# Optimization experiments

Measured on AMD Instinct MI355X. Metric: run time of the kernel, lower is better.

## Reference

```python
import jax, jax.numpy as jnp
import numpy as np

B, F, P, H = 8192, 32, 512, 256
EPS_W = 1e-8   # weight-normalization eps from _normalize_weights
EPS_LN = 1e-5  # torch LayerNorm default eps


def setup_inputs() -> dict:
    key = jax.random.key(0)
    k0, k1, k2, k3, k4 = jax.random.split(key, 5)
    phys = jax.random.normal(k0, (B, F, P), dtype=jnp.float32)
    ratios = jax.random.uniform(k1, (B, F), dtype=jnp.float32)
    lengths = jax.random.randint(k2, (B,), 1, F + 1, dtype=jnp.int32)
    ln_gamma = jnp.ones((P,), jnp.float32)
    ln_beta = jnp.zeros((P,), jnp.float32)
    lim1 = float(np.sqrt(6.0 / (P + H)))  # xavier_uniform
    W1 = jax.random.uniform(k3, (H, P), jnp.float32, -lim1, lim1)
    b1 = jnp.zeros((H,), jnp.float32)
    lim2 = float(np.sqrt(6.0 / (H + 1)))
    W2 = jax.random.uniform(k4, (1, H), jnp.float32, -lim2, lim2)
    b2 = jnp.zeros((1,), jnp.float32)
    return dict(phys=phys, ratios=ratios, lengths=lengths,
                ln_gamma=ln_gamma, ln_beta=ln_beta,
                W1=W1, b1=b1, W2=W2, b2=b2)


def reference(phys, ratios, lengths, ln_gamma, ln_beta, W1, b1, W2, b2):
    # Ragged weighted mix: mask padded fragments, normalize weights per sample.
    mask = (jnp.arange(F)[None, :] < lengths[:, None]).astype(phys.dtype)  # [B,F]
    w = ratios * mask
    w = w / (jnp.sum(w, axis=-1, keepdims=True) + EPS_W)
    mix = jnp.einsum('bf,bfp->bp', w, phys)  # [B,P]
    # Head: LayerNorm(P) -> Linear(P,H) -> ReLU -> Linear(H,1)
    mu = jnp.mean(mix, axis=-1, keepdims=True)
    var = jnp.mean((mix - mu) ** 2, axis=-1, keepdims=True)
    xn = (mix - mu) * jax.lax.rsqrt(var + EPS_LN) * ln_gamma + ln_beta
    h = jax.nn.relu(xn @ W1.T + b1)  # [B,H]
    y = h @ W2.T + b2                # [B,1]
    return jnp.nan_to_num(y)
```

## Files before the change

kernel.cpp:

```cpp
#include <hip/hip_runtime.h>
#include <math.h>

#define BB 8192
#define FF 32
#define PP 512
#define HH 256
#define S  16

__global__ void transpose_w1(const float* __restrict__ W1, float* __restrict__ W1T) {
    int p = blockIdx.x;
    int j = threadIdx.x;
    W1T[((p >> 2) * HH + j) * 4 + (p & 3)] = W1[j * PP + p];
}

__global__ __launch_bounds__(256, 2)
void fused_physchem(const float* __restrict__ phys,
                    const float* __restrict__ ratios,
                    const int*   __restrict__ lengths,
                    const float* __restrict__ gamma,
                    const float* __restrict__ beta,
                    const float* __restrict__ W1T,
                    const float* __restrict__ b1,
                    const float* __restrict__ W2,
                    const float* __restrict__ b2,
                    float* __restrict__ out) {
    constexpr int PADP = PP + 4;
    __shared__ float wts[S][FF];
    __shared__ int   slen[S];
    __shared__ __align__(16) float xn[S][PADP];
    __shared__ float red[4][8][2];

    const int tid  = threadIdx.x;
    const int wave = tid >> 6;
    const int lane = tid & 63;
    const int b0   = blockIdx.x * S;

    {
        int g = tid >> 5;
        int f = tid & 31;
        #pragma unroll
        for (int rep = 0; rep < 2; ++rep) {
            int s = g + 8 * rep;
            int len = lengths[b0 + s];
            float r = ratios[(b0 + s) * FF + f];
            float w = (f < len) ? r : 0.0f;
            float sum = w;
            #pragma unroll
            for (int m = 16; m >= 1; m >>= 1) sum += __shfl_xor(sum, m, 32);
            wts[s][f] = w / (sum + 1e-8f);
            if (f == 0) slen[s] = len;
        }
    }
    __syncthreads();

    const int pt = tid & 127;
    const int sh = tid >> 7;
    float4 mixacc[8];
    {
        const float4* phys4 = (const float4*)phys;
        #pragma unroll
        for (int k = 0; k < 8; ++k) {
            const int s   = 2 * k + sh;
            const int len = slen[s];
            const float4* row = phys4 + (size_t)(b0 + s) * FF * (PP / 4) + pt;
            float4 a = make_float4(0.f, 0.f, 0.f, 0.f);
            #pragma unroll 8
            for (int f = 0; f < len; ++f) {
                float  w = wts[s][f];
                float4 v = row[(size_t)f * (PP / 4)];
                a.x += w * v.x; a.y += w * v.y;
                a.z += w * v.z; a.w += w * v.w;
            }
            mixacc[k] = a;
        }
    }

    #pragma unroll
    for (int k = 0; k < 8; ++k) {
        float4 a = mixacc[k];
        float sum = a.x + a.y + a.z + a.w;
        float sq  = a.x * a.x + a.y * a.y + a.z * a.z + a.w * a.w;
        #pragma unroll
        for (int m = 32; m >= 1; m >>= 1) {
            sum += __shfl_xor(sum, m, 64);
            sq  += __shfl_xor(sq,  m, 64);
        }
        if (lane == 0) { red[wave][k][0] = sum; red[wave][k][1] = sq; }
    }
    __syncthreads();
    {
        float4 g  = ((const float4*)gamma)[pt];
        float4 be = ((const float4*)beta)[pt];
        const int wbase = sh * 2;
        #pragma unroll
        for (int k = 0; k < 8; ++k) {
            const int s = 2 * k + sh;
            float sum = red[wbase][k][0] + red[wbase + 1][k][0];
            float sq  = red[wbase][k][1] + red[wbase + 1][k][1];
            float mu  = sum * (1.0f / PP);
            float var = sq * (1.0f / PP) - mu * mu;
            float inv = rsqrtf(var + 1e-5f);
            float4 a = mixacc[k];
            float4 o;
            o.x = (a.x - mu) * inv * g.x + be.x;
            o.y = (a.y - mu) * inv * g.y + be.y;
            o.z = (a.z - mu) * inv * g.z + be.z;
            o.w = (a.w - mu) * inv * g.w + be.w;
            *(float4*)&xn[s][4 * pt] = o;
        }
    }
    __syncthreads();

    float hacc[4][4];
    #pragma unroll
    for (int t = 0; t < 4; ++t)
        #pragma unroll
        for (int jj = 0; jj < 4; ++jj) hacc[t][jj] = 0.f;
    {
        const int sb = wave * 4;
        const float4* W1T4 = (const float4*)W1T;
        for (int c = 0; c < PP / 4; ++c) {
            float4 wv[4];
            #pragma unroll
            for (int jj = 0; jj < 4; ++jj)
                wv[jj] = W1T4[c * HH + lane + 64 * jj];
            #pragma unroll
            for (int t = 0; t < 4; ++t) {
                float4 xv = *(const float4*)&xn[sb + t][4 * c];
                #pragma unroll
                for (int jj = 0; jj < 4; ++jj)
                    hacc[t][jj] += wv[jj].x * xv.x + wv[jj].y * xv.y
                                 + wv[jj].z * xv.z + wv[jj].w * xv.w;
            }
        }
    }
    {
        const int sb = wave * 4;
        float b1v[4], w2v[4];
        #pragma unroll
        for (int jj = 0; jj < 4; ++jj) {
            b1v[jj] = b1[lane + 64 * jj];
            w2v[jj] = W2[lane + 64 * jj];
        }
        float b2v = b2[0];
        #pragma unroll
        for (int t = 0; t < 4; ++t) {
            float v = 0.f;
            #pragma unroll
            for (int jj = 0; jj < 4; ++jj) {
                float h = hacc[t][jj] + b1v[jj];
                h = h > 0.f ? h : 0.f;
                v += h * w2v[jj];
            }
            #pragma unroll
            for (int m = 32; m >= 1; m >>= 1) v += __shfl_xor(v, m, 64);
            if (lane == 0) {
                float y = v + b2v;
                if (isnan(y)) y = 0.f;
                else if (isinf(y)) y = (y > 0.f) ? 3.402823466e38f : -3.402823466e38f;
                out[b0 + sb + t] = y;
            }
        }
    }
}

extern "C" void kernel_launch(void* const* d_in, const int* in_sizes, int n_in,
                              void* d_out, int out_size, void* d_ws, size_t ws_size,
                              hipStream_t stream) {
    const float* phys    = (const float*)d_in[0];
    const float* ratios  = (const float*)d_in[1];
    const int*   lengths = (const int*)  d_in[2];
    const float* gamma   = (const float*)d_in[3];
    const float* beta    = (const float*)d_in[4];
    const float* W1      = (const float*)d_in[5];
    const float* b1      = (const float*)d_in[6];
    const float* W2      = (const float*)d_in[7];
    const float* b2      = (const float*)d_in[8];
    float* out = (float*)d_out;
    float* W1T = (float*)d_ws;

    transpose_w1<<<dim3(PP), dim3(HH), 0, stream>>>(W1, W1T);
    fused_physchem<<<dim3(BB / S), dim3(256), 0, stream>>>(
        phys, ratios, lengths, gamma, beta, W1T, b1, W2, b2, out);
}
```

Before: 689.0 us.

## Split fused kernel into mix+LayerNorm and MLP kernels via global intermediate

Splits the single fused kernel into two launches. The first is a mix+LayerNorm kernel with one wave per sample, reading two float4s per lane per fragment, broadcasting weights by shuffle and reducing without shared memory. The second is an MLP kernel that reads the normalized rows back from a global device buffer. This is meant to raise occupancy and memory parallelism in the bandwidth-bound phys streaming phase, where the old kernel had each thread loop serially over 8 samples. The cost is an extra 16 MB write and read of the intermediate, one more launch, and static device globals in place of the provided workspace.

```diff
diff --git a/kernel.cpp b/kernel.cpp
--- a/kernel.cpp
+++ b/kernel.cpp
@@ -5,109 +5,102 @@
 #define FF 32
 #define PP 512
 #define HH 256
-#define S  16
+#define SB 16
 
-__global__ void transpose_w1(const float* __restrict__ W1, float* __restrict__ W1T) {
+__device__ float g_w1t[PP * HH];
+__device__ float g_xn[(size_t)BB * PP];
+
+__global__ void transpose_w1(const float* __restrict__ W1) {
     int p = blockIdx.x;
     int j = threadIdx.x;
-    W1T[((p >> 2) * HH + j) * 4 + (p & 3)] = W1[j * PP + p];
+    g_w1t[((p >> 2) * HH + j) * 4 + (p & 3)] = W1[j * PP + p];
+}
+
+__global__ __launch_bounds__(256, 4)
+void mix_ln(const float* __restrict__ phys,
+            const float* __restrict__ ratios,
+            const int*   __restrict__ lengths,
+            const float* __restrict__ gamma,
+            const float* __restrict__ beta) {
+    const int wave = threadIdx.x >> 6;
+    const int lane = threadIdx.x & 63;
+    const int b    = blockIdx.x * 4 + wave;
+
+    const int len = lengths[b];
+
+    float w;
+    {
+        float r = ratios[b * FF + (lane & 31)];
+        w = ((lane & 31) < len) ? r : 0.0f;
+        float s = w;
+        #pragma unroll
+        for (int m = 16; m >= 1; m >>= 1) s += __shfl_xor(s, m, 32);
+        w = w / (s + 1e-8f);
+    }
+
+    const float4* p4 = (const float4*)phys + (size_t)b * FF * (PP / 4);
+    float4 a0 = make_float4(0.f, 0.f, 0.f, 0.f);
+    float4 a1 = make_float4(0.f, 0.f, 0.f, 0.f);
+    #pragma unroll 4
+    for (int f = 0; f < len; ++f) {
+        float  wf = __shfl(w, f);
+        float4 v0 = p4[f * (PP / 4) + lane];
+        float4 v1 = p4[f * (PP / 4) + 64 + lane];
+        a0.x = fmaf(wf, v0.x, a0.x); a0.y = fmaf(wf, v0.y, a0.y);
+        a0.z = fmaf(wf, v0.z, a0.z); a0.w = fmaf(wf, v0.w, a0.w);
+        a1.x = fmaf(wf, v1.x, a1.x); a1.y = fmaf(wf, v1.y, a1.y);
+        a1.z = fmaf(wf, v1.z, a1.z); a1.w = fmaf(wf, v1.w, a1.w);
+    }
+
+    float sum = a0.x + a0.y + a0.z + a0.w + a1.x + a1.y + a1.z + a1.w;
+    float sq  = a0.x * a0.x + a0.y * a0.y + a0.z * a0.z + a0.w * a0.w
+              + a1.x * a1.x + a1.y * a1.y + a1.z * a1.z + a1.w * a1.w;
+    #pragma unroll
+    for (int m = 32; m >= 1; m >>= 1) {
+        sum += __shfl_xor(sum, m, 64);
+        sq  += __shfl_xor(sq,  m, 64);
+    }
+    float mu  = sum * (1.0f / PP);
+    float var = sq * (1.0f / PP) - mu * mu;
+    float inv = rsqrtf(var + 1e-5f);
+
+    float4 g0  = ((const float4*)gamma)[lane];
+    float4 g1  = ((const float4*)gamma)[64 + lane];
+    float4 be0 = ((const float4*)beta)[lane];
+    float4 be1 = ((const float4*)beta)[64 + lane];
+    float4 o0, o1;
+    o0.x = (a0.x - mu) * inv * g0.x + be0.x;
+    o0.y = (a0.y - mu) * inv * g0.y + be0.y;
+    o0.z = (a0.z - mu) * inv * g0.z + be0.z;
+    o0.w = (a0.w - mu) * inv * g0.w + be0.w;
+    o1.x = (a1.x - mu) * inv * g1.x + be1.x;
+    o1.y = (a1.y - mu) * inv * g1.y + be1.y;
+    o1.z = (a1.z - mu) * inv * g1.z + be1.z;
+    o1.w = (a1.w - mu) * inv * g1.w + be1.w;
+
+    float4* dst = (float4*)(g_xn + (size_t)b * PP);
+    dst[lane]      = o0;
+    dst[64 + lane] = o1;
 }
 
 __global__ __launch_bounds__(256, 2)
-void fused_physchem(const float* __restrict__ phys,
-                    const float* __restrict__ ratios,
-                    const int*   __restrict__ lengths,
-                    const float* __restrict__ gamma,
-                    const float* __restrict__ beta,
-                    const float* __restrict__ W1T,
-                    const float* __restrict__ b1,
-                    const float* __restrict__ W2,
-                    const float* __restrict__ b2,
-                    float* __restrict__ out) {
-    constexpr int PADP = PP + 4;
-    __shared__ float wts[S][FF];
-    __shared__ int   slen[S];
-    __shared__ __align__(16) float xn[S][PADP];
-    __shared__ float red[4][8][2];
+void mlp(const float* __restrict__ b1,
+         const float* __restrict__ W2,
+         const float* __restrict__ b2,
+         float*       __restrict__ out) {
+    __shared__ __align__(16) float xs[SB][PP];
 
     const int tid  = threadIdx.x;
     const int wave = tid >> 6;
     const int lane = tid & 63;
-    const int b0   = blockIdx.x * S;
+    const int b0   = blockIdx.x * SB;
 
     {
-        int g = tid >> 5;
-        int f = tid & 31;
+        const float4* src = (const float4*)(g_xn + (size_t)b0 * PP);
+        float4* dst = (float4*)xs;
         #pragma unroll
-        for (int rep = 0; rep < 2; ++rep) {
-            int s = g + 8 * rep;
-            int len = lengths[b0 + s];
-            float r = ratios[(b0 + s) * FF + f];
-            float w = (f < len) ? r : 0.0f;
-            float sum = w;
-            #pragma unroll
-            for (int m = 16; m >= 1; m >>= 1) sum += __shfl_xor(sum, m, 32);
-            wts[s][f] = w / (sum + 1e-8f);
-            if (f == 0) slen[s] = len;
-        }
-    }
-    __syncthreads();
-
-    const int pt = tid & 127;
-    const int sh = tid >> 7;
-    float4 mixacc[8];
-    {
-        const float4* phys4 = (const float4*)phys;
-        #pragma unroll
-        for (int k = 0; k < 8; ++k) {
-            const int s   = 2 * k + sh;
-            const int len = slen[s];
-            const float4* row = phys4 + (size_t)(b0 + s) * FF * (PP / 4) + pt;
-            float4 a = make_float4(0.f, 0.f, 0.f, 0.f);
-            #pragma unroll 8
-            for (int f = 0; f < len; ++f) {
-                float  w = wts[s][f];
-                float4 v = row[(size_t)f * (PP / 4)];
-                a.x += w * v.x; a.y += w * v.y;
-                a.z += w * v.z; a.w += w * v.w;
-            }
-            mixacc[k] = a;
-        }
-    }
-
-    #pragma unroll
-    for (int k = 0; k < 8; ++k) {
-        float4 a = mixacc[k];
-        float sum = a.x + a.y + a.z + a.w;
-        float sq  = a.x * a.x + a.y * a.y + a.z * a.z + a.w * a.w;
-        #pragma unroll
-        for (int m = 32; m >= 1; m >>= 1) {
-            sum += __shfl_xor(sum, m, 64);
-            sq  += __shfl_xor(sq,  m, 64);
-        }
-        if (lane == 0) { red[wave][k][0] = sum; red[wave][k][1] = sq; }
-    }
-    __syncthreads();
-    {
-        float4 g  = ((const float4*)gamma)[pt];
-        float4 be = ((const float4*)beta)[pt];
-        const int wbase = sh * 2;
-        #pragma unroll
-        for (int k = 0; k < 8; ++k) {
-            const int s = 2 * k + sh;
-            float sum = red[wbase][k][0] + red[wbase + 1][k][0];
-            float sq  = red[wbase][k][1] + red[wbase + 1][k][1];
-            float mu  = sum * (1.0f / PP);
-            float var = sq * (1.0f / PP) - mu * mu;
-            float inv = rsqrtf(var + 1e-5f);
-            float4 a = mixacc[k];
-            float4 o;
-            o.x = (a.x - mu) * inv * g.x + be.x;
-            o.y = (a.y - mu) * inv * g.y + be.y;
-            o.z = (a.z - mu) * inv * g.z + be.z;
-            o.w = (a.w - mu) * inv * g.w + be.w;
-            *(float4*)&xn[s][4 * pt] = o;
-        }
+        for (int i = 0; i < SB * PP / 4 / 256; ++i)
+            dst[tid + 256 * i] = src[tid + 256 * i];
     }
     __syncthreads();
 
@@ -118,7 +111,7 @@
         for (int jj = 0; jj < 4; ++jj) hacc[t][jj] = 0.f;
     {
         const int sb = wave * 4;
-        const float4* W1T4 = (const float4*)W1T;
+        const float4* W1T4 = (const float4*)g_w1t;
         for (int c = 0; c < PP / 4; ++c) {
             float4 wv[4];
             #pragma unroll
@@ -126,7 +119,7 @@
                 wv[jj] = W1T4[c * HH + lane + 64 * jj];
             #pragma unroll
             for (int t = 0; t < 4; ++t) {
-                float4 xv = *(const float4*)&xn[sb + t][4 * c];
+                float4 xv = *(const float4*)&xs[sb + t][4 * c];
                 #pragma unroll
                 for (int jj = 0; jj < 4; ++jj)
                     hacc[t][jj] += wv[jj].x * xv.x + wv[jj].y * xv.y
@@ -177,9 +170,9 @@
     const float* W2      = (const float*)d_in[7];
     const float* b2      = (const float*)d_in[8];
     float* out = (float*)d_out;
-    float* W1T = (float*)d_ws;
+    (void)d_ws; (void)ws_size;
 
-    transpose_w1<<<dim3(PP), dim3(HH), 0, stream>>>(W1, W1T);
-    fused_physchem<<<dim3(BB / S), dim3(256), 0, stream>>>(
-        phys, ratios, lengths, gamma, beta, W1T, b1, W2, b2, out);
+    transpose_w1<<<dim3(PP), dim3(HH), 0, stream>>>(W1);
+    mix_ln<<<dim3(BB / 4), dim3(256), 0, stream>>>(phys, ratios, lengths, gamma, beta);
+    mlp<<<dim3(BB / SB), dim3(256), 0, stream>>>(b1, W2, b2, out);
 }
```

Result: slower. 704.9 us (+2.3%).
